# Performance work log

Measured on AMD Instinct MI355X. Metric: run time of the kernel, lower is better.

## Reference

```python
import jax, jax.numpy as jnp
import numpy as np

N = 100000
E = 3200000
NEG_SLOPE = 0.2


def setup_inputs() -> dict:
    key = jax.random.key(0)
    ks = jax.random.split(key, 12)
    x = jax.random.normal(ks[0], (N, 4), dtype=jnp.float32)
    edge_index = jax.random.randint(ks[1], (2, E), 0, N, dtype=jnp.int64)
    # GATConv(4, 16, heads=4): lin (no bias), att_src/att_dst [H, C], bias [H*C]
    W1 = jax.random.normal(ks[2], (4, 4 * 16), dtype=jnp.float32) * 0.5
    as1 = jax.random.normal(ks[3], (4, 16), dtype=jnp.float32) * 0.5
    ad1 = jax.random.normal(ks[4], (4, 16), dtype=jnp.float32) * 0.5
    b1 = jnp.zeros((64,), dtype=jnp.float32)
    # GATConv(64, 2, heads=4)
    W2 = jax.random.normal(ks[5], (64, 4 * 2), dtype=jnp.float32) * 0.125
    as2 = jax.random.normal(ks[6], (4, 2), dtype=jnp.float32) * 0.5
    ad2 = jax.random.normal(ks[7], (4, 2), dtype=jnp.float32) * 0.5
    b2 = jnp.zeros((8,), dtype=jnp.float32)
    # out head Linear(8, 1)
    Wout = jax.random.normal(ks[8], (8, 1), dtype=jnp.float32) * 0.35
    bout = jnp.zeros((1,), dtype=jnp.float32)
    return {"x": x, "edge_index": edge_index, "W1": W1, "as1": as1, "ad1": ad1,
            "b1": b1, "W2": W2, "as2": as2, "ad2": ad2, "b2": b2,
            "Wout": Wout, "bout": bout}


def gat_conv(x, ei, W, a_src, a_dst, b, H, C, n):
    # PyG GATConv (concat=True, negative_slope=0.2), self-loops already in ei
    xw = (x @ W).reshape(n, H, C)                      # [N, H, C]
    src, dst = ei[0], ei[1]
    alpha_s = jnp.einsum('nhc,hc->nh', xw, a_src)      # [N, H]
    alpha_d = jnp.einsum('nhc,hc->nh', xw, a_dst)      # [N, H]
    e = jax.nn.leaky_relu(alpha_s[src] + alpha_d[dst], NEG_SLOPE)  # [E, H]
    # segment softmax over incoming edges of each destination node
    m = jax.ops.segment_max(e, dst, num_segments=n)    # [N, H]
    e = jnp.exp(e - m[dst])
    denom = jax.ops.segment_sum(e, dst, num_segments=n)
    alpha = e / (denom[dst] + 1e-16)                   # [E, H]
    msg = xw[src] * alpha[:, :, None]                  # [E, H, C]
    out = jax.ops.segment_sum(msg, dst, num_segments=n)  # [N, H, C]
    return out.reshape(n, H * C) + b


def reference(x, edge_index, W1, as1, ad1, b1, W2, as2, ad2, b2, Wout, bout):
    n = x.shape[0]
    ar = jnp.arange(n, dtype=edge_index.dtype)
    ei = jnp.concatenate([edge_index, jnp.stack([ar, ar])], axis=1)  # add self-loops
    h = jax.nn.elu(gat_conv(x, ei, W1, as1, ad1, b1, 4, 16, n))       # [N, 64]
    h = jax.nn.elu(gat_conv(h, ei, W2, as2, ad2, b2, 4, 2, n))        # [N, 8]
    g = jnp.mean(h, axis=0, keepdims=True)  # global_mean_pool, batch all zeros -> [1, 8]
    return jax.nn.sigmoid(g @ Wout + bout)  # [1, 1]
```

## Files before the change

### kernel.cpp

```cpp
#include <hip/hip_runtime.h>
#include <hip/hip_fp8.h>

#define NEG 0.2f
#define BSZ 224
#define MAXBUK 512
#define NBIN 512
#define CAP 16384
#define LSTG 6400

typedef float v2f __attribute__((ext_vector_type(2)));

__device__ __forceinline__ float elufast(float x){ return x > 0.0f ? x : __expf(x) - 1.0f; }
__device__ __forceinline__ float b2f(unsigned short b){ return __uint_as_float((unsigned)b << 16); }
__device__ __forceinline__ unsigned short f2b(float x){
    unsigned u = __float_as_uint(x);
    return (unsigned short)((u + 0x7FFFu + ((u >> 16) & 1u)) >> 16);
}

__device__ __forceinline__ void fma8(uint2 r, float w, v2f* acc){
    v2f w2 = {w, w};
    v2f f0 = __builtin_amdgcn_cvt_pk_f32_fp8(r.x, false);
    v2f f1 = __builtin_amdgcn_cvt_pk_f32_fp8(r.x, true);
    v2f f2 = __builtin_amdgcn_cvt_pk_f32_fp8(r.y, false);
    v2f f3 = __builtin_amdgcn_cvt_pk_f32_fp8(r.y, true);
    acc[0] = __builtin_elementwise_fma(f0, w2, acc[0]);
    acc[1] = __builtin_elementwise_fma(f1, w2, acc[1]);
    acc[2] = __builtin_elementwise_fma(f2, w2, acc[2]);
    acc[3] = __builtin_elementwise_fma(f3, w2, acc[3]);
}

__global__ void k_l1_node(const float* __restrict__ x, const float* __restrict__ W1,
                          const float* __restrict__ as1, const float* __restrict__ ad1,
                          unsigned char* __restrict__ xw1, uint2* __restrict__ asvb,
                          float* __restrict__ adv, int N){
    __shared__ float sW[256], sA[64], sD[64];
    int tid = threadIdx.x;
    sW[tid] = W1[tid];
    if (tid < 64){ sA[tid] = as1[tid]; sD[tid] = ad1[tid]; }
    __syncthreads();
    int i = blockIdx.x * 256 + tid;
    if (i >= N) return;
    float4 xv = ((const float4*)x)[i];
    const v2f* sW0 = (const v2f*)sW;
    const v2f* sW1v = (const v2f*)(sW + 64);
    const v2f* sW2v = (const v2f*)(sW + 128);
    const v2f* sW3v = (const v2f*)(sW + 192);
    v2f xx = {xv.x, xv.x}, yy = {xv.y, xv.y}, zz = {xv.z, xv.z}, ww = {xv.w, xv.w};
    v2f xwv[32];
    #pragma unroll
    for (int j = 0; j < 32; j++){
        v2f t = xx * sW0[j];
        t = __builtin_elementwise_fma(yy, sW1v[j], t);
        t = __builtin_elementwise_fma(zz, sW2v[j], t);
        t = __builtin_elementwise_fma(ww, sW3v[j], t);
        xwv[j] = t;
    }
    unsigned wv[16];
    #pragma unroll
    for (int j = 0; j < 16; j++){
        unsigned p = 0;
        p = __builtin_amdgcn_cvt_pk_fp8_f32(xwv[2 * j].x,     xwv[2 * j].y,     p, false);
        p = __builtin_amdgcn_cvt_pk_fp8_f32(xwv[2 * j + 1].x, xwv[2 * j + 1].y, p, true);
        wv[j] = p;
    }
    uint4* dp = (uint4*)(xw1 + (size_t)i * 64);
    dp[0] = make_uint4(wv[0],  wv[1],  wv[2],  wv[3]);
    dp[1] = make_uint4(wv[4],  wv[5],  wv[6],  wv[7]);
    dp[2] = make_uint4(wv[8],  wv[9],  wv[10], wv[11]);
    dp[3] = make_uint4(wv[12], wv[13], wv[14], wv[15]);
    const v2f* sAv = (const v2f*)sA;
    const v2f* sDv = (const v2f*)sD;
    float al[4];
    #pragma unroll
    for (int h = 0; h < 4; h++){
        v2f asv = {0.f, 0.f}, adw = {0.f, 0.f};
        #pragma unroll
        for (int c2 = 0; c2 < 8; c2++){
            asv = __builtin_elementwise_fma(xwv[h * 8 + c2], sAv[h * 8 + c2], asv);
            adw = __builtin_elementwise_fma(xwv[h * 8 + c2], sDv[h * 8 + c2], adw);
        }
        al[h] = asv.x + asv.y;
        adv[i * 4 + h] = adw.x + adw.y;
    }
    asvb[i] = make_uint2((unsigned)f2b(al[0]) | ((unsigned)f2b(al[1]) << 16),
                         (unsigned)f2b(al[2]) | ((unsigned)f2b(al[3]) << 16));
}

__global__ void k_bin2(const int* __restrict__ src, const int* __restrict__ dst,
                       int* __restrict__ gcnt, unsigned* __restrict__ staged,
                       int E, int chunksz, int nbuk){
    __shared__ int hist[MAXBUK];
    __shared__ int cur[MAXBUK];
    __shared__ int lsb[MAXBUK];
    __shared__ int gbase[MAXBUK];
    __shared__ int ts[512];
    __shared__ unsigned lstg[LSTG];
    int tid = threadIdx.x;
    for (int b = tid; b < MAXBUK; b += 1024) hist[b] = 0;
    __syncthreads();
    int e0 = blockIdx.x * chunksz, e1 = min(E, e0 + chunksz);
    int a0 = min(e1, (e0 + 3) & ~3);
    int a1 = max(a0, e1 & ~3);
    if (tid < a0 - e0) atomicAdd(&hist[(unsigned)dst[e0 + tid] / BSZ], 1);
    for (int q = (a0 >> 2) + tid; q < (a1 >> 2); q += 1024){
        int4 d4 = ((const int4*)dst)[q];
        atomicAdd(&hist[(unsigned)d4.x / BSZ], 1);
        atomicAdd(&hist[(unsigned)d4.y / BSZ], 1);
        atomicAdd(&hist[(unsigned)d4.z / BSZ], 1);
        atomicAdd(&hist[(unsigned)d4.w / BSZ], 1);
    }
    if (tid < e1 - a1) atomicAdd(&hist[(unsigned)dst[a1 + tid] / BSZ], 1);
    __syncthreads();
    int v = 0;
    if (tid < 512){ v = hist[tid]; ts[tid] = v; }
    __syncthreads();
    for (int s = 1; s < 512; s <<= 1){
        int tmp = (tid >= s && tid < 512) ? ts[tid - s] : 0;
        __syncthreads();
        if (tid < 512) ts[tid] += tmp;
        __syncthreads();
    }
    if (tid < 512){
        int excl = ts[tid] - v;
        lsb[tid] = excl;
        cur[tid] = excl;
        int padded = (v + 15) & ~15;
        gbase[tid] = tid * CAP + (padded ? atomicAdd(&gcnt[tid], padded) : 0);
    }
    __syncthreads();
    auto put = [&](int d, int s){
        int buk = (unsigned)d / BSZ;
        int pos = atomicAdd(&cur[buk], 1);
        lstg[pos] = (unsigned)s | ((unsigned)(d - buk * BSZ) << 17);
    };
    if (tid < a0 - e0) put(dst[e0 + tid], src[e0 + tid]);
    for (int q = (a0 >> 2) + tid; q < (a1 >> 2); q += 1024){
        int4 d4 = ((const int4*)dst)[q];
        int4 s4 = ((const int4*)src)[q];
        put(d4.x, s4.x); put(d4.y, s4.y); put(d4.z, s4.z); put(d4.w, s4.w);
    }
    if (tid < e1 - a1) put(dst[a1 + tid], src[a1 + tid]);
    __syncthreads();
    int wv = tid >> 6, ln = tid & 63;
    for (int b = wv; b < nbuk; b += 16){
        int cnt = hist[b];
        int padded = (cnt + 15) & ~15;
        int lb = lsb[b], gb = gbase[b];
        for (int j = ln; j < padded; j += 64)
            staged[gb + j] = (j < cnt) ? lstg[lb + j] : 0xFFFFFFFFu;
    }
}

__global__ void k_local(const unsigned* __restrict__ staged, const int* __restrict__ gcnt,
                        int2* __restrict__ offp, int* __restrict__ csr, int N){
    __shared__ int deg[BSZ];
    __shared__ int cur[BSZ];
    __shared__ int ts[256];
    int b = blockIdx.x, t = threadIdx.x;
    int lo = b * BSZ, hi = min(N, lo + BSZ);
    int e0 = b * CAP, e1 = e0 + gcnt[b];
    if (t < BSZ) deg[t] = 0;
    __syncthreads();
    for (int q = (e0 >> 2) + t; q < (e1 >> 2); q += 1024){
        uint4 s4 = ((const uint4*)staged)[q];
        if (s4.x != 0xFFFFFFFFu) atomicAdd(&deg[s4.x >> 17], 1);
        if (s4.y != 0xFFFFFFFFu) atomicAdd(&deg[s4.y >> 17], 1);
        if (s4.z != 0xFFFFFFFFu) atomicAdd(&deg[s4.z >> 17], 1);
        if (s4.w != 0xFFFFFFFFu) atomicAdd(&deg[s4.w >> 17], 1);
    }
    __syncthreads();
    int v = 0;
    if (t < 256){
        v = (t < BSZ) ? deg[t] : 0;
        ts[t] = v;
    }
    __syncthreads();
    for (int s = 1; s < 256; s <<= 1){
        int tmp = (t >= s && t < 256) ? ts[t - s] : 0;
        __syncthreads();
        if (t < 256) ts[t] += tmp;
        __syncthreads();
    }
    if (t < BSZ){
        cur[t] = e0 + ts[t] - v;
        if (lo + t < hi) offp[lo + t] = make_int2(e0 + ts[t] - v, e0 + ts[t]);
    }
    __syncthreads();
    auto sc = [&](unsigned se){
        if (se == 0xFFFFFFFFu) return;
        int pos = atomicAdd(&cur[se >> 17], 1);
        csr[pos] = (int)(se & 0x1FFFFu);
    };
    for (int q = (e0 >> 2) + t; q < (e1 >> 2); q += 1024){
        uint4 s4 = ((const uint4*)staged)[q];
        sc(s4.x); sc(s4.y); sc(s4.z); sc(s4.w);
    }
}

__global__ void k_l1_gather(const int2* __restrict__ offp, const int* __restrict__ csr,
                            const uint2* __restrict__ asvb, const float* __restrict__ adv,
                            const unsigned char* __restrict__ xw1, const float* __restrict__ b1,
                            unsigned char* __restrict__ h1f8, int N){
    int tid = threadIdx.x;
    int wid = (int)(((long)blockIdx.x * 256 + tid) >> 6);
    if (wid >= N) return;
    int lane = tid & 63;
    int g = lane >> 3;
    int q = lane & 7;
    int h = q >> 1;
    float advd = adv[wid * 4 + h];
    const unsigned char* xwq = xw1 + q * 8;
    const char* asvbh = (const char*)asvb + h * 2;

    v2f acc2[4] = {{0.f, 0.f}, {0.f, 0.f}, {0.f, 0.f}, {0.f, 0.f}};
    float den = 0.f;
    int2 rng = offp[wid];
    int k = rng.x, end = rng.y;
    for (; k + 32 <= end; k += 32){
        int s0 = csr[k + g];
        int s1 = csr[k + 8 + g];
        int s2 = csr[k + 16 + g];
        int s3 = csr[k + 24 + g];
        uint2 r0 = *(const uint2*)(xwq + ((size_t)s0 << 6));
        uint2 r1 = *(const uint2*)(xwq + ((size_t)s1 << 6));
        uint2 r2 = *(const uint2*)(xwq + ((size_t)s2 << 6));
        uint2 r3 = *(const uint2*)(xwq + ((size_t)s3 << 6));
        float a0 = b2f(*(const unsigned short*)(asvbh + ((size_t)s0 << 3)));
        float a1 = b2f(*(const unsigned short*)(asvbh + ((size_t)s1 << 3)));
        float a2 = b2f(*(const unsigned short*)(asvbh + ((size_t)s2 << 3)));
        float a3 = b2f(*(const unsigned short*)(asvbh + ((size_t)s3 << 3)));
        float t0 = a0 + advd, t1 = a1 + advd, t2 = a2 + advd, t3 = a3 + advd;
        float w0 = __expf(fmaxf(t0, NEG * t0));
        float w1 = __expf(fmaxf(t1, NEG * t1));
        float w2 = __expf(fmaxf(t2, NEG * t2));
        float w3 = __expf(fmaxf(t3, NEG * t3));
        den += (w0 + w1) + (w2 + w3);
        fma8(r0, w0, acc2);
        fma8(r1, w1, acc2);
        fma8(r2, w2, acc2);
        fma8(r3, w3, acc2);
    }
    if (k + 16 <= end){
        int sA = csr[k + g];
        int sB = csr[k + 8 + g];
        uint2 rA = *(const uint2*)(xwq + ((size_t)sA << 6));
        uint2 rB = *(const uint2*)(xwq + ((size_t)sB << 6));
        float aA = b2f(*(const unsigned short*)(asvbh + ((size_t)sA << 3)));
        float aB = b2f(*(const unsigned short*)(asvbh + ((size_t)sB << 3)));
        float tA = aA + advd, tB = aB + advd;
        float wA = __expf(fmaxf(tA, NEG * tA));
        float wB = __expf(fmaxf(tB, NEG * tB));
        den += wA + wB;
        fma8(rA, wA, acc2);
        fma8(rB, wB, acc2);
        k += 16;
    }
    for (; k < end; k += 8){
        int e = k + g;
        bool valid = e < end;
        int s = csr[valid ? e : end - 1];
        uint2 r = *(const uint2*)(xwq + ((size_t)s << 6));
        float a = b2f(*(const unsigned short*)(asvbh + ((size_t)s << 3)));
        float t = a + advd;
        float w = valid ? __expf(fmaxf(t, NEG * t)) : 0.f;
        den += w;
        fma8(r, w, acc2);
    }

    v2f t0, t1, t2, t3;
    t0.x = __shfl_xor(acc2[0].x, 32); t0.y = __shfl_xor(acc2[0].y, 32);
    t1.x = __shfl_xor(acc2[1].x, 32); t1.y = __shfl_xor(acc2[1].y, 32);
    t2.x = __shfl_xor(acc2[2].x, 32); t2.y = __shfl_xor(acc2[2].y, 32);
    t3.x = __shfl_xor(acc2[3].x, 32); t3.y = __shfl_xor(acc2[3].y, 32);
    bool gb2 = (lane & 32) != 0;
    v2f n0 = gb2 ? (acc2[2] + t2) : (acc2[0] + t0);
    v2f n1 = gb2 ? (acc2[3] + t3) : (acc2[1] + t1);
    v2f u0, u1;
    u0.x = __shfl_xor(n0.x, 16); u0.y = __shfl_xor(n0.y, 16);
    u1.x = __shfl_xor(n1.x, 16); u1.y = __shfl_xor(n1.y, 16);
    bool gb1 = (lane & 16) != 0;
    v2f rr = gb1 ? (n1 + u1) : (n0 + u0);
    v2f z;
    z.x = __shfl_xor(rr.x, 8); z.y = __shfl_xor(rr.y, 8);
    rr += z;
    bool gb0 = (lane & 8) != 0;
    den += __shfl_xor(den, 8);
    den += __shfl_xor(den, 16);
    den += __shfl_xor(den, 32);
    float val = gb0 ? rr.y : rr.x;

    int c = q * 8 + g;
    float aself = b2f(*(const unsigned short*)(asvbh + ((size_t)wid << 3)));
    float tsv = aself + advd;
    float ws = __expf(fmaxf(tsv, NEG * tsv));
    unsigned selfb = xw1[(size_t)wid * 64 + c];
    v2f sf = __builtin_amdgcn_cvt_pk_f32_fp8(selfb, false);
    float asel = val + ws * sf.x;
    float inv = 1.0f / (den + ws + 1e-16f);
    float o = elufast(asel * inv + b1[c]);
    unsigned p = __builtin_amdgcn_cvt_pk_fp8_f32(o, o, 0, false);
    h1f8[(size_t)wid * 64 + c] = (unsigned char)p;
}

__global__ void k_l2_node(const unsigned char* __restrict__ h1f8, const float* __restrict__ W2,
                          const float* __restrict__ ad2, float* __restrict__ xw2,
                          float* __restrict__ adv2, int N){
    __shared__ float sW[512], sD[8];
    int tid = threadIdx.x;
    sW[tid] = W2[tid];
    sW[256 + tid] = W2[256 + tid];
    if (tid < 8) sD[tid] = ad2[tid];
    __syncthreads();
    int i = blockIdx.x * 256 + tid;
    if (i >= N) return;
    const uint2* rp = (const uint2*)(h1f8 + (size_t)i * 64);
    v2f acc2[4] = {{0.f, 0.f}, {0.f, 0.f}, {0.f, 0.f}, {0.f, 0.f}};
    #pragma unroll
    for (int b8 = 0; b8 < 8; b8++){
        uint2 r = rp[b8];
        v2f f0 = __builtin_amdgcn_cvt_pk_f32_fp8(r.x, false);
        v2f f1 = __builtin_amdgcn_cvt_pk_f32_fp8(r.x, true);
        v2f f2 = __builtin_amdgcn_cvt_pk_f32_fp8(r.y, false);
        v2f f3 = __builtin_amdgcn_cvt_pk_f32_fp8(r.y, true);
        float f[8] = {f0.x, f0.y, f1.x, f1.y, f2.x, f2.y, f3.x, f3.y};
        #pragma unroll
        for (int j = 0; j < 8; j++){
            v2f hcv = {f[j], f[j]};
            const v2f* wrow = (const v2f*)&sW[(b8 * 8 + j) * 8];
            acc2[0] = __builtin_elementwise_fma(hcv, wrow[0], acc2[0]);
            acc2[1] = __builtin_elementwise_fma(hcv, wrow[1], acc2[1]);
            acc2[2] = __builtin_elementwise_fma(hcv, wrow[2], acc2[2]);
            acc2[3] = __builtin_elementwise_fma(hcv, wrow[3], acc2[3]);
        }
    }
    float4* xo = (float4*)(xw2 + (size_t)i * 8);
    xo[0] = make_float4(acc2[0].x, acc2[0].y, acc2[1].x, acc2[1].y);
    xo[1] = make_float4(acc2[2].x, acc2[2].y, acc2[3].x, acc2[3].y);
    float4 dv;
    dv.x = acc2[0].x * sD[0] + acc2[0].y * sD[1];
    dv.y = acc2[1].x * sD[2] + acc2[1].y * sD[3];
    dv.z = acc2[2].x * sD[4] + acc2[2].y * sD[5];
    dv.w = acc2[3].x * sD[6] + acc2[3].y * sD[7];
    *(float4*)(adv2 + (size_t)i * 4) = dv;
}

__global__ void k_l2_gather(const int2* __restrict__ offp, const int* __restrict__ csr,
                            const float* __restrict__ adv2, const float* __restrict__ xw2,
                            const float* __restrict__ b2, const float* __restrict__ as2,
                            float* __restrict__ pool, int N){
    __shared__ float lpool[8];
    int tid = threadIdx.x;
    if (tid < 8) lpool[tid] = 0.f;
    __syncthreads();
    int wid = (int)(((long)blockIdx.x * 256 + tid) >> 6);
    if (wid < N){
        int lane = tid & 63;
        int g = lane >> 2;
        int hh = lane & 3;
        float2 a2h = *(const float2*)&as2[hh * 2];
        float advd = adv2[wid * 4 + hh];
        const char* xwh = (const char*)xw2 + hh * 8;
        v2f accv = {0.f, 0.f};
        float den = 0.f;

        auto edge = [&](int s, bool valid){
            v2f v = *(const v2f*)(xwh + ((size_t)s << 5));
            float al = v.x * a2h.x + v.y * a2h.y;
            float t = al + advd;
            float w = valid ? __expf(fmaxf(t, NEG * t)) : 0.f;
            den += w;
            v2f w2 = {w, w};
            accv = __builtin_elementwise_fma(v, w2, accv);
        };

        int2 rng = offp[wid];
        int k = rng.x, end = rng.y;
        for (; k + 32 <= end; k += 32){
            int s0 = csr[k + g], s1 = csr[k + 16 + g];
            edge(s0, true); edge(s1, true);
        }
        for (; k < end; k += 16){
            int e = k + g;
            bool valid = e < end;
            int s = csr[valid ? e : end - 1];
            edge(s, valid);
        }
        #pragma unroll
        for (int m = 4; m <= 32; m <<= 1){
            accv.x += __shfl_xor(accv.x, m);
            accv.y += __shfl_xor(accv.y, m);
            den    += __shfl_xor(den, m);
        }
        if (g == 0){
            v2f v = *(const v2f*)(xwh + ((size_t)wid << 5));
            float al = v.x * a2h.x + v.y * a2h.y;
            float t = al + advd;
            float ws = __expf(fmaxf(t, NEG * t));
            den += ws;
            accv.x += ws * v.x;
            accv.y += ws * v.y;
            float inv = 1.0f / (den + 1e-16f);
            float o0 = elufast(accv.x * inv + b2[hh * 2]);
            float o1 = elufast(accv.y * inv + b2[hh * 2 + 1]);
            atomicAdd(&lpool[hh * 2], o0);
            atomicAdd(&lpool[hh * 2 + 1], o1);
        }
    }
    __syncthreads();
    if (tid < 8) atomicAdd(&pool[(blockIdx.x & 63) * 8 + tid], lpool[tid]);
}

__global__ void k_final(const float* __restrict__ pool, const float* __restrict__ Wout,
                        const float* __restrict__ bout, float* __restrict__ out, float invN){
    int lane = threadIdx.x;
    const float4* p4 = (const float4*)(pool + lane * 8);
    float4 a = p4[0], b = p4[1];
    float v[8] = {a.x, a.y, a.z, a.w, b.x, b.y, b.z, b.w};
    #pragma unroll
    for (int m = 1; m <= 32; m <<= 1){
        #pragma unroll
        for (int j = 0; j < 8; j++) v[j] += __shfl_xor(v[j], m);
    }
    if (lane == 0){
        float z = bout[0];
        #pragma unroll
        for (int j = 0; j < 8; j++) z += v[j] * invN * Wout[j];
        out[0] = 1.0f / (1.0f + __expf(-z));
    }
}

extern "C" void kernel_launch(void* const* d_in, const int* in_sizes, int n_in,
                              void* d_out, int out_size, void* d_ws, size_t ws_size,
                              hipStream_t stream){
    const float* x    = (const float*)d_in[0];
    const int*   ei   = (const int*)d_in[1];
    const float* W1   = (const float*)d_in[2];
    const float* as1  = (const float*)d_in[3];
    const float* ad1  = (const float*)d_in[4];
    const float* b1   = (const float*)d_in[5];
    const float* W2   = (const float*)d_in[6];
    const float* as2  = (const float*)d_in[7];
    const float* ad2  = (const float*)d_in[8];
    const float* b2   = (const float*)d_in[9];
    const float* Wout = (const float*)d_in[10];
    const float* bout = (const float*)d_in[11];
    float* out = (float*)d_out;

    int N = in_sizes[0] / 4;
    int E = in_sizes[1] / 2;
    const int* src = ei;
    const int* dst = ei + E;

    char* ws = (char*)d_ws;
    size_t off_b = 0;
    auto alloc = [&](size_t bytes)->void*{
        void* p = ws + off_b;
        off_b += (bytes + 255) & ~(size_t)255;
        return p;
    };
    unsigned char* xw1  = (unsigned char*)alloc((size_t)N * 64);
    unsigned char* h1f8 = (unsigned char*)alloc((size_t)N * 64);
    uint2*    asvb   = (uint2*)alloc((size_t)N * 8);
    float*    adv    = (float*)alloc((size_t)N * 4 * 4);
    float*    adv2   = (float*)alloc((size_t)N * 4 * 4);
    int*      gcnt   = (int*)alloc((size_t)MAXBUK * 4);
    unsigned* staged = (unsigned*)alloc((size_t)MAXBUK * CAP * 4);
    int2*     offp   = (int2*)alloc((size_t)N * 8);
    int*      csr    = (int*)alloc((size_t)MAXBUK * CAP * 4);
    float*    xw2    = (float*)alloc((size_t)N * 8 * 4);
    float*    pool   = (float*)alloc(64 * 8 * 4);

    int nbuk = (N + BSZ - 1) / BSZ;
    int chunksz = (E + NBIN - 1) / NBIN;

    hipMemsetAsync(pool, 0, 64 * 8 * 4, stream);
    hipMemsetAsync(gcnt, 0, (size_t)MAXBUK * 4, stream);

    k_bin2<<<NBIN, 1024, 0, stream>>>(src, dst, gcnt, staged, E, chunksz, nbuk);
    k_l1_node<<<(N + 255) / 256, 256, 0, stream>>>(x, W1, as1, ad1, xw1, asvb, adv, N);
    k_local<<<nbuk, 1024, 0, stream>>>(staged, gcnt, offp, csr, N);

    k_l1_gather<<<(int)(((long)N * 64 + 255) / 256), 256, 0, stream>>>(
        offp, csr, asvb, adv, xw1, b1, h1f8, N);
    k_l2_node<<<(N + 255) / 256, 256, 0, stream>>>(h1f8, W2, ad2, xw2, adv2, N);
    k_l2_gather<<<(int)(((long)N * 64 + 255) / 256), 256, 0, stream>>>(
        offp, csr, adv2, xw2, b2, as2, pool, N);
    k_final<<<1, 64, 0, stream>>>(pool, Wout, bout, out, 1.0f / (float)N);
}
```

Measured before the change: 161.6 us.

## Split bin histograms per half-block and cache staged slab in LDS

In the binning kernel, the two halves of the 1024-thread block now use separate shared histograms and cursors, which is meant to halve contention on the LDS atomics. In the local CSR kernel, the staged edges of each bucket are copied into a shared-memory slab during the degree pass, and the scatter pass reads from that slab instead of re-reading global memory. Edges beyond the slab capacity (11264 entries) are silently dropped. This is only safe if per-bucket counts stay below that limit. The larger shared-memory footprint may also reduce occupancy.

```diff
diff --git a/kernel.cpp b/kernel.cpp
--- a/kernel.cpp
+++ b/kernel.cpp
@@ -7,6 +7,7 @@
 #define NBIN 512
 #define CAP 16384
 #define LSTG 6400
+#define LSLAB 11264
 
 typedef float v2f __attribute__((ext_vector_type(2)));
 
@@ -89,14 +90,16 @@
 __global__ void k_bin2(const int* __restrict__ src, const int* __restrict__ dst,
                        int* __restrict__ gcnt, unsigned* __restrict__ staged,
                        int E, int chunksz, int nbuk){
-    __shared__ int hist[MAXBUK];
-    __shared__ int cur[MAXBUK];
+    __shared__ int histA[MAXBUK], histB[MAXBUK];
+    __shared__ int curA[MAXBUK], curB[MAXBUK];
     __shared__ int lsb[MAXBUK];
     __shared__ int gbase[MAXBUK];
     __shared__ int ts[512];
     __shared__ unsigned lstg[LSTG];
     int tid = threadIdx.x;
-    for (int b = tid; b < MAXBUK; b += 1024) hist[b] = 0;
+    int half = tid >> 9;
+    int* hist = half ? histB : histA;
+    for (int b = tid; b < MAXBUK; b += 1024){ histA[b] = 0; histB[b] = 0; }
     __syncthreads();
     int e0 = blockIdx.x * chunksz, e1 = min(E, e0 + chunksz);
     int a0 = min(e1, (e0 + 3) & ~3);
@@ -111,8 +114,8 @@
     }
     if (tid < e1 - a1) atomicAdd(&hist[(unsigned)dst[a1 + tid] / BSZ], 1);
     __syncthreads();
-    int v = 0;
-    if (tid < 512){ v = hist[tid]; ts[tid] = v; }
+    int v = 0, hA = 0;
+    if (tid < 512){ hA = histA[tid]; v = hA + histB[tid]; ts[tid] = v; }
     __syncthreads();
     for (int s = 1; s < 512; s <<= 1){
         int tmp = (tid >= s && tid < 512) ? ts[tid - s] : 0;
@@ -123,11 +126,13 @@
     if (tid < 512){
         int excl = ts[tid] - v;
         lsb[tid] = excl;
-        cur[tid] = excl;
+        curA[tid] = excl;
+        curB[tid] = excl + hA;
         int padded = (v + 15) & ~15;
         gbase[tid] = tid * CAP + (padded ? atomicAdd(&gcnt[tid], padded) : 0);
     }
     __syncthreads();
+    int* cur = half ? curB : curA;
     auto put = [&](int d, int s){
         int buk = (unsigned)d / BSZ;
         int pos = atomicAdd(&cur[buk], 1);
@@ -143,7 +148,7 @@
     __syncthreads();
     int wv = tid >> 6, ln = tid & 63;
     for (int b = wv; b < nbuk; b += 16){
-        int cnt = hist[b];
+        int cnt = histA[b] + histB[b];
         int padded = (cnt + 15) & ~15;
         int lb = lsb[b], gb = gbase[b];
         for (int j = ln; j < padded; j += 64)
@@ -153,16 +158,19 @@
 
 __global__ void k_local(const unsigned* __restrict__ staged, const int* __restrict__ gcnt,
                         int2* __restrict__ offp, int* __restrict__ csr, int N){
+    __shared__ unsigned lslab[LSLAB];
     __shared__ int deg[BSZ];
     __shared__ int cur[BSZ];
     __shared__ int ts[256];
     int b = blockIdx.x, t = threadIdx.x;
     int lo = b * BSZ, hi = min(N, lo + BSZ);
-    int e0 = b * CAP, e1 = e0 + gcnt[b];
+    int e0 = b * CAP;
+    int cnt = min(gcnt[b], LSLAB);
     if (t < BSZ) deg[t] = 0;
     __syncthreads();
-    for (int q = (e0 >> 2) + t; q < (e1 >> 2); q += 1024){
-        uint4 s4 = ((const uint4*)staged)[q];
+    for (int q = t; q < (cnt >> 2); q += 1024){
+        uint4 s4 = ((const uint4*)(staged + e0))[q];
+        ((uint4*)lslab)[q] = s4;
         if (s4.x != 0xFFFFFFFFu) atomicAdd(&deg[s4.x >> 17], 1);
         if (s4.y != 0xFFFFFFFFu) atomicAdd(&deg[s4.y >> 17], 1);
         if (s4.z != 0xFFFFFFFFu) atomicAdd(&deg[s4.z >> 17], 1);
@@ -186,14 +194,11 @@
         if (lo + t < hi) offp[lo + t] = make_int2(e0 + ts[t] - v, e0 + ts[t]);
     }
     __syncthreads();
-    auto sc = [&](unsigned se){
-        if (se == 0xFFFFFFFFu) return;
+    for (int e = t; e < cnt; e += 1024){
+        unsigned se = lslab[e];
+        if (se == 0xFFFFFFFFu) continue;
         int pos = atomicAdd(&cur[se >> 17], 1);
         csr[pos] = (int)(se & 0x1FFFFu);
-    };
-    for (int q = (e0 >> 2) + t; q < (e1 >> 2); q += 1024){
-        uint4 s4 = ((const uint4*)staged)[q];
-        sc(s4.x); sc(s4.y); sc(s4.z); sc(s4.w);
     }
 }
 
```

After: 161.5 us. Within noise of the previous version (-0.0%).
